# Kernel tuning notes

Hardware: AMD Instinct MI355X
Metric: run time of the kernel (lower is better)

Reference implementation:

```python
import jax, jax.numpy as jnp
import numpy as np


def setup_inputs() -> dict:
    key = jax.random.key(0)
    k1, k2, k3, k4 = jax.random.split(key, 4)
    B, T, C, H = 16, 2048, 384, 64
    x = jax.random.normal(k1, (B, T, C), dtype=jnp.float32)
    Wq = jax.random.normal(k2, (C, H), dtype=jnp.float32) * (1.0 / np.sqrt(C))
    Wk = jax.random.normal(k3, (C, H), dtype=jnp.float32) * (1.0 / np.sqrt(C))
    Wv = jax.random.normal(k4, (C, H), dtype=jnp.float32) * (1.0 / np.sqrt(C))
    return {"x": x, "Wq": Wq, "Wk": Wk, "Wv": Wv}


def reference(x, Wq, Wk, Wv):
    # x: [B, T, C]; Wq/Wk/Wv: [C, H]
    T = x.shape[1]
    H = Wk.shape[1]
    q = jnp.einsum('btc,ch->bth', x, Wq)
    k = jnp.einsum('btc,ch->bth', x, Wk)
    v = jnp.einsum('btc,ch->bth', x, Wv)
    scale = 1.0 / jnp.sqrt(jnp.asarray(H, dtype=x.dtype))
    wei = jnp.einsum('bth,bsh->bts', q, k) * scale  # [B, T, T]
    causal = jnp.tril(jnp.ones((T, T), dtype=bool))
    wei = jnp.where(causal, wei, -jnp.inf)
    attn = jax.nn.softmax(wei, axis=-1)
    # dropout p=0 -> identity
    out = jnp.einsum('bts,bsh->bth', attn, v)  # [B, T, H]
    return out
```

## Files before the change

kernel.cpp:

```cpp
#include <hip/hip_runtime.h>
#include <hip/hip_bf16.h>

#define B_ 16
#define T_ 2048
#define C_ 384
#define H_ 64

typedef __attribute__((ext_vector_type(8))) short short8;
typedef __attribute__((ext_vector_type(4))) short short4_t;
typedef __attribute__((ext_vector_type(4))) float floatx4;

static __device__ __forceinline__ short f2bf(float f) {
    unsigned u = __builtin_bit_cast(unsigned, f);
    u += 0x7FFF + ((u >> 16) & 1);
    return (short)(u >> 16);
}

__global__ void wt_kernel(const float* __restrict__ Wq, const float* __restrict__ Wk,
                          const float* __restrict__ Wv, short* __restrict__ wt2) {
    int idx = blockIdx.x * 256 + threadIdx.x;
    if (idx >= 12 * 12 * 512) return;
    int f = idx >> 9, within = idx & 511;
    int lane = within >> 3, jj = within & 7;
    int nt16 = f / 12, kc32 = f - nt16 * 12;
    int mat = nt16 >> 2, w = nt16 & 3;
    int quad = lane >> 4, l16 = lane & 15;
    int h = w * 16 + l16;
    int c = kc32 * 32 + quad * 8 + jj;
    const float* W = (mat == 0) ? Wq : ((mat == 1) ? Wk : Wv);
    wt2[idx] = f2bf(W[c * H_ + h]);
}

__global__ __launch_bounds__(256) void qkv_kernel(
        const float* __restrict__ x, const short* __restrict__ wt2,
        short* __restrict__ qo, short* __restrict__ ko, short* __restrict__ vto) {
    __shared__ short xs[32 * 392];

    int b = blockIdx.y, t0 = blockIdx.x * 32;
    int tid = threadIdx.x;

    const float* src = x + (size_t)(b * T_ + t0) * C_;
    for (int i = 0; i < 12; i++) {
        int chunk = i * 256 + tid;
        int row = chunk / 96, off = (chunk % 96) * 4;
        float4 f = *(const float4*)&src[row * 384 + off];
        short4_t s4;
        s4.x = f2bf(f.x); s4.y = f2bf(f.y); s4.z = f2bf(f.z); s4.w = f2bf(f.w);
        *(short4_t*)&xs[row * 392 + off] = s4;
    }
    __syncthreads();

    int w = tid >> 6, lane = tid & 63, quad = lane >> 4, l16 = lane & 15;

    floatx4 acc[2][3];
    for (int mt = 0; mt < 2; mt++)
        for (int j = 0; j < 3; j++) acc[mt][j] = (floatx4)0.0f;

    for (int kc = 0; kc < 384; kc += 32) {
        int kc32 = kc >> 5;
        short8 a0 = *(const short8*)&xs[l16 * 392 + kc + quad * 8];
        short8 a1 = *(const short8*)&xs[(16 + l16) * 392 + kc + quad * 8];
        for (int j = 0; j < 3; j++) {
            short8 bf = *(const short8*)&wt2[(((j * 4 + w) * 12) + kc32) * 512 + lane * 8];
            acc[0][j] = __builtin_amdgcn_mfma_f32_16x16x32_bf16(a0, bf, acc[0][j], 0, 0, 0);
            acc[1][j] = __builtin_amdgcn_mfma_f32_16x16x32_bf16(a1, bf, acc[1][j], 0, 0, 0);
        }
    }
    __syncthreads();

    {
        int h = w * 16 + l16;
        for (int j = 0; j < 3; j++)
            for (int mt = 0; mt < 2; mt++)
                for (int r = 0; r < 4; r++) {
                    int tl = mt * 16 + quad * 4 + r;
                    short bv = f2bf(acc[mt][j][r]);
                    if (j == 0)      xs[tl * 72 + h] = bv;
                    else if (j == 1) xs[2304 + tl * 72 + h] = bv;
                    else             xs[4608 + h * 40 + tl] = bv;
                }
    }
    __syncthreads();

    {
        int row = tid >> 3, off = (tid & 7) * 8;
        *(short8*)&qo[(size_t)(b * T_ + t0 + row) * H_ + off] = *(const short8*)&xs[row * 72 + off];
        *(short8*)&ko[(size_t)(b * T_ + t0 + row) * H_ + off] = *(const short8*)&xs[2304 + row * 72 + off];
    }
    {
        int h = tid >> 2, off = (tid & 3) * 8;
        *(short8*)&vto[(size_t)(b * H_ + h) * T_ + t0 + off] = *(const short8*)&xs[4608 + h * 40 + off];
    }
}

__global__ __launch_bounds__(256) void attn_seg_kernel(
        const short* __restrict__ q, const short* __restrict__ k,
        const short* __restrict__ vt, float* __restrict__ slots) {
    __shared__ short ks[64 * 72];
    __shared__ short vs[64 * 72];
    __shared__ short ps[128 * 72];

    int b = blockIdx.y, fid = blockIdx.x, nslot = gridDim.x;
    int tt = 0, cum = 0;
    while (cum + ((2 * tt + 5) >> 2) <= fid) { cum += (2 * tt + 5) >> 2; tt++; }
    int nk = 2 * tt + 2;
    int k0 = (fid - cum) * 4;
    int k1 = min(k0 + 4, nk);

    int tid = threadIdx.x, w = tid >> 6, lane = tid & 63, quad = lane >> 4, l16 = lane & 15;
    int trow0 = tt * 128 + w * 32;

    short8 aq[2][2];
    for (int mt = 0; mt < 2; mt++) {
        const short* qrow = q + (size_t)(b * T_ + trow0 + mt * 16 + l16) * H_;
        aq[mt][0] = *(const short8*)&qrow[quad * 8];
        aq[mt][1] = *(const short8*)&qrow[32 + quad * 8];
    }

    floatx4 o[2][4];
    float lp[2][4];
    for (int mt = 0; mt < 2; mt++)
        for (int i = 0; i < 4; i++) { o[mt][i] = (floatx4)0.0f; lp[mt][i] = 0.f; }

    const short* kb0 = k + (size_t)b * T_ * H_;
    const short* vtb = vt + (size_t)b * H_ * T_;
    short* psw = ps + w * 32 * 72;

    int srow = tid >> 3, soff = (tid & 7) * 8;
    const float C1 = 0.125f * 1.44269504f;
    const float C2 = 12.0f * 1.44269504f;

    for (int st = k0; st < k1; st++) {
        int s0 = st * 64;
        const short* kg = kb0 + (size_t)s0 * H_;
        const short* vg = vtb + s0;
        *(short8*)&ks[srow * 72 + soff]        = *(const short8*)&kg[srow * H_ + soff];
        *(short8*)&ks[(srow + 32) * 72 + soff] = *(const short8*)&kg[(srow + 32) * H_ + soff];
        *(short8*)&vs[srow * 72 + soff]        = *(const short8*)&vg[(size_t)srow * T_ + soff];
        *(short8*)&vs[(srow + 32) * 72 + soff] = *(const short8*)&vg[(size_t)(srow + 32) * T_ + soff];
        __syncthreads();

        floatx4 sacc[2][4];
        for (int mt = 0; mt < 2; mt++)
            for (int nt = 0; nt < 4; nt++) sacc[mt][nt] = (floatx4)0.0f;
        for (int nt = 0; nt < 4; nt++) {
            short8 bk0 = *(const short8*)&ks[(nt * 16 + l16) * 72 + quad * 8];
            short8 bk1 = *(const short8*)&ks[(nt * 16 + l16) * 72 + 32 + quad * 8];
            sacc[0][nt] = __builtin_amdgcn_mfma_f32_16x16x32_bf16(aq[0][0], bk0, sacc[0][nt], 0, 0, 0);
            sacc[0][nt] = __builtin_amdgcn_mfma_f32_16x16x32_bf16(aq[0][1], bk1, sacc[0][nt], 0, 0, 0);
            sacc[1][nt] = __builtin_amdgcn_mfma_f32_16x16x32_bf16(aq[1][0], bk0, sacc[1][nt], 0, 0, 0);
            sacc[1][nt] = __builtin_amdgcn_mfma_f32_16x16x32_bf16(aq[1][1], bk1, sacc[1][nt], 0, 0, 0);
        }

        bool diag = (st >= 2 * tt);
        for (int mt = 0; mt < 2; mt++)
            for (int nt = 0; nt < 4; nt++) {
                int s_idx = s0 + nt * 16 + l16;
                for (int r = 0; r < 4; r++) {
                    float p = exp2f(fmaf(sacc[mt][nt][r], C1, -C2));
                    if (diag && (s_idx > trow0 + mt * 16 + quad * 4 + r)) p = 0.0f;
                    lp[mt][r] += p;
                    psw[(mt * 16 + quad * 4 + r) * 72 + nt * 16 + l16] = f2bf(p);
                }
            }

        short8 ap[2][2];
        for (int mt = 0; mt < 2; mt++) {
            ap[mt][0] = *(const short8*)&psw[(mt * 16 + l16) * 72 + quad * 8];
            ap[mt][1] = *(const short8*)&psw[(mt * 16 + l16) * 72 + 32 + quad * 8];
        }
        for (int nh = 0; nh < 4; nh++) {
            short8 bv0 = *(const short8*)&vs[(nh * 16 + l16) * 72 + quad * 8];
            short8 bv1 = *(const short8*)&vs[(nh * 16 + l16) * 72 + 32 + quad * 8];
            o[0][nh] = __builtin_amdgcn_mfma_f32_16x16x32_bf16(ap[0][0], bv0, o[0][nh], 0, 0, 0);
            o[0][nh] = __builtin_amdgcn_mfma_f32_16x16x32_bf16(ap[0][1], bv1, o[0][nh], 0, 0, 0);
            o[1][nh] = __builtin_amdgcn_mfma_f32_16x16x32_bf16(ap[1][0], bv0, o[1][nh], 0, 0, 0);
            o[1][nh] = __builtin_amdgcn_mfma_f32_16x16x32_bf16(ap[1][1], bv1, o[1][nh], 0, 0, 0);
        }
        __syncthreads();
    }

    for (int d = 1; d < 16; d <<= 1)
        for (int mt = 0; mt < 2; mt++)
            for (int r = 0; r < 4; r++)
                lp[mt][r] += __shfl_xor(lp[mt][r], d, 16);

    float* slot = slots + ((size_t)b * nslot + fid) * 8320;
    for (int mt = 0; mt < 2; mt++)
        for (int nh = 0; nh < 4; nh++)
            for (int r = 0; r < 4; r++)
                slot[(w * 32 + mt * 16 + quad * 4 + r) * 64 + nh * 16 + l16] = o[mt][nh][r];
    if (l16 == 0)
        for (int mt = 0; mt < 2; mt++)
            for (int r = 0; r < 4; r++)
                slot[8192 + w * 32 + mt * 16 + quad * 4 + r] = lp[mt][r];
}

__global__ __launch_bounds__(256) void combine_kernel(
        const float* __restrict__ slots, int nslot, float* __restrict__ out) {
    int b = blockIdx.y, tt = blockIdx.x;
    int nseg = (2 * tt + 5) >> 2;
    int cum = 0;
    for (int i = 0; i < tt; i++) cum += (2 * i + 5) >> 2;
    const float* base = slots + ((size_t)b * nslot + cum) * 8320;

    int tid = threadIdx.x;
    int row = tid >> 1, c0 = (tid & 1) * 32;
    float4 acc[8] = {};
    float lsum = 0.f;
    for (int s = 0; s < nseg; s++) {
        const float* sp = base + (size_t)s * 8320;
        for (int i = 0; i < 8; i++) {
            float4 v = *(const float4*)&sp[row * 64 + c0 + i * 4];
            acc[i].x += v.x; acc[i].y += v.y; acc[i].z += v.z; acc[i].w += v.w;
        }
        lsum += sp[8192 + row];
    }
    float inv = 1.0f / lsum;
    float* op = out + (size_t)(b * T_ + tt * 128 + row) * H_ + c0;
    for (int i = 0; i < 8; i++) {
        float4 v;
        v.x = acc[i].x * inv; v.y = acc[i].y * inv;
        v.z = acc[i].z * inv; v.w = acc[i].w * inv;
        *(float4*)&op[i * 4] = v;
    }
}

template<bool DIAG>
static __device__ __forceinline__ void attn_step(
        int s0, int t0w, int quad, int l16,
        const short* __restrict__ kbase, const short* __restrict__ vtb,
        short8 aq0, short8 aq1, short* __restrict__ psw,
        floatx4 (&o)[4], float (&lpart)[4]) {
    floatx4 sacc[4];
    for (int nt = 0; nt < 4; nt++) sacc[nt] = (floatx4)0.0f;
    for (int nt = 0; nt < 4; nt++) {
        short8 bk0 = *(const short8*)&kbase[(nt * 16 + l16) * H_ + quad * 8];
        short8 bk1 = *(const short8*)&kbase[(nt * 16 + l16) * H_ + 32 + quad * 8];
        sacc[nt] = __builtin_amdgcn_mfma_f32_16x16x32_bf16(aq0, bk0, sacc[nt], 0, 0, 0);
        sacc[nt] = __builtin_amdgcn_mfma_f32_16x16x32_bf16(aq1, bk1, sacc[nt], 0, 0, 0);
    }
    const float C1 = 0.125f * 1.44269504f;
    const float C2 = 12.0f * 1.44269504f;
    for (int nt = 0; nt < 4; nt++) {
        int s_idx = s0 + nt * 16 + l16;
        for (int r = 0; r < 4; r++) {
            float p = exp2f(fmaf(sacc[nt][r], C1, -C2));
            if (DIAG && (s_idx > t0w + quad * 4 + r)) p = 0.0f;
            lpart[r] += p;
            psw[(quad * 4 + r) * 72 + nt * 16 + l16] = f2bf(p);
        }
    }
    short8 ap0 = *(const short8*)&psw[l16 * 72 + quad * 8];
    short8 ap1 = *(const short8*)&psw[l16 * 72 + 32 + quad * 8];
    for (int nh = 0; nh < 4; nh++) {
        short8 bv0 = *(const short8*)&vtb[(size_t)(nh * 16 + l16) * T_ + s0 + quad * 8];
        short8 bv1 = *(const short8*)&vtb[(size_t)(nh * 16 + l16) * T_ + s0 + 32 + quad * 8];
        o[nh] = __builtin_amdgcn_mfma_f32_16x16x32_bf16(ap0, bv0, o[nh], 0, 0, 0);
        o[nh] = __builtin_amdgcn_mfma_f32_16x16x32_bf16(ap1, bv1, o[nh], 0, 0, 0);
    }
}

__global__ __launch_bounds__(256) void attn_kernel(
        const short* __restrict__ q, const short* __restrict__ k,
        const short* __restrict__ vt, float* __restrict__ out) {
    __shared__ short ps[4 * 16 * 72];

    int b = blockIdx.y;
    int g = ((int)blockIdx.x + 4 * (b & 7)) & 31;
    int tt = (b < 8) ? g : 31 - g;
    int t0 = tt * 64;
    int tid = threadIdx.x, w = tid >> 6, lane = tid & 63, quad = lane >> 4, l16 = lane & 15;
    int t0w = t0 + w * 16;

    const short* qrow = q + (size_t)(b * T_ + t0w + l16) * H_;
    short8 aq0 = *(const short8*)&qrow[quad * 8];
    short8 aq1 = *(const short8*)&qrow[32 + quad * 8];

    floatx4 o[4];
    for (int nh = 0; nh < 4; nh++) o[nh] = (floatx4)0.0f;
    float lpart[4] = {0.f, 0.f, 0.f, 0.f};

    const short* kb0 = k + (size_t)b * T_ * H_;
    const short* vtb = vt + (size_t)b * H_ * T_;
    short* psw = ps + w * 16 * 72;

    for (int st = 0; st < tt; st++)
        attn_step<false>(st * 64, t0w, quad, l16, kb0 + (size_t)st * 64 * H_,
                         vtb, aq0, aq1, psw, o, lpart);
    attn_step<true>(tt * 64, t0w, quad, l16, kb0 + (size_t)tt * 64 * H_,
                    vtb, aq0, aq1, psw, o, lpart);

    for (int d = 1; d < 16; d <<= 1)
        for (int r = 0; r < 4; r++)
            lpart[r] += __shfl_xor(lpart[r], d, 16);

    for (int nh = 0; nh < 4; nh++)
        for (int r = 0; r < 4; r++) {
            int t = t0w + quad * 4 + r;
            out[(size_t)(b * T_ + t) * H_ + nh * 16 + l16] = o[nh][r] / lpart[r];
        }
}

extern "C" void kernel_launch(void* const* d_in, const int* in_sizes, int n_in,
                              void* d_out, int out_size, void* d_ws, size_t ws_size,
                              hipStream_t stream) {
    const float* x  = (const float*)d_in[0];
    const float* Wq = (const float*)d_in[1];
    const float* Wk = (const float*)d_in[2];
    const float* Wv = (const float*)d_in[3];

    char* ws = (char*)d_ws;
    short* qb  = (short*)(ws);
    short* kb  = (short*)(ws + (size_t)4 * 1024 * 1024);
    short* vtb = (short*)(ws + (size_t)8 * 1024 * 1024);
    short* wtb = (short*)(ws + (size_t)12 * 1024 * 1024);
    float* slots = (float*)(ws + (size_t)12 * 1024 * 1024 + 256 * 1024);
    size_t base_need = (size_t)12 * 1024 * 1024 + 256 * 1024;

    wt_kernel<<<dim3(288), dim3(256), 0, stream>>>(Wq, Wk, Wv, wtb);
    qkv_kernel<<<dim3(T_ / 32, B_), dim3(256), 0, stream>>>(x, wtb, qb, kb, vtb);

    float* out = (float*)d_out;
    const int NSLOT = 72;
    if (ws_size >= base_need + (size_t)B_ * NSLOT * 8320 * sizeof(float)) {
        attn_seg_kernel<<<dim3(NSLOT, B_), dim3(256), 0, stream>>>(qb, kb, vtb, slots);
        combine_kernel<<<dim3(T_ / 128, B_), dim3(256), 0, stream>>>(slots, NSLOT, out);
    } else {
        attn_kernel<<<dim3(T_ / 64, B_), dim3(256), 0, stream>>>(qb, kb, vtb, out);
    }
}
```

Measured before the change: 143.3 us.

## Double-buffer K/V tiles and store split-K partials as bf16

The segmented attention kernel now prefetches the next K/V tile into registers while computing the current one, then writes it into a second shared-memory buffer, removing one barrier per iteration. The per-warp P staging buffer is shrunk to 16 rows and reused per m-tile. Partial outputs in the slot buffer are stored as bf16 through shared memory with coalesced 16-byte stores instead of fp32, halving slot traffic for the combine kernel. This trades extra registers and some precision in the partial sums for less memory traffic and better load/compute overlap.

Measured after the change: 140.6 us. About the same (-1.9%).

```diff
diff --git a/kernel.cpp b/kernel.cpp
--- a/kernel.cpp
+++ b/kernel.cpp
@@ -14,6 +14,9 @@
     unsigned u = __builtin_bit_cast(unsigned, f);
     u += 0x7FFF + ((u >> 16) & 1);
     return (short)(u >> 16);
+}
+static __device__ __forceinline__ float bf2f(short s) {
+    return __builtin_bit_cast(float, ((unsigned)(unsigned short)s) << 16);
 }
 
 __global__ void wt_kernel(const float* __restrict__ Wq, const float* __restrict__ Wk,
@@ -93,12 +96,15 @@
     }
 }
 
+#define KVSZ (64 * 72)
+#define SLOT_BYTES (16384 + 512)
+
 __global__ __launch_bounds__(256) void attn_seg_kernel(
         const short* __restrict__ q, const short* __restrict__ k,
         const short* __restrict__ vt, float* __restrict__ slots) {
-    __shared__ short ks[64 * 72];
-    __shared__ short vs[64 * 72];
-    __shared__ short ps[128 * 72];
+    __shared__ short ks[2 * KVSZ];
+    __shared__ short vs[2 * KVSZ];
+    __shared__ short ps[4 * 16 * 72];
 
     int b = blockIdx.y, fid = blockIdx.x, nslot = gridDim.x;
     int tt = 0, cum = 0;
@@ -124,28 +130,48 @@
 
     const short* kb0 = k + (size_t)b * T_ * H_;
     const short* vtb = vt + (size_t)b * H_ * T_;
-    short* psw = ps + w * 32 * 72;
+    short* psw = ps + w * 16 * 72;
 
     int srow = tid >> 3, soff = (tid & 7) * 8;
     const float C1 = 0.125f * 1.44269504f;
     const float C2 = 12.0f * 1.44269504f;
 
+    {
+        const short* kg = kb0 + (size_t)k0 * 64 * H_;
+        const short* vg = vtb + k0 * 64;
+        short8 a = *(const short8*)&kg[srow * H_ + soff];
+        short8 c = *(const short8*)&kg[(srow + 32) * H_ + soff];
+        short8 d = *(const short8*)&vg[(size_t)srow * T_ + soff];
+        short8 e = *(const short8*)&vg[(size_t)(srow + 32) * T_ + soff];
+        *(short8*)&ks[srow * 72 + soff] = a;
+        *(short8*)&ks[(srow + 32) * 72 + soff] = c;
+        *(short8*)&vs[srow * 72 + soff] = d;
+        *(short8*)&vs[(srow + 32) * 72 + soff] = e;
+    }
+    __syncthreads();
+
+    int p = 0;
     for (int st = k0; st < k1; st++) {
+        bool more = (st + 1 < k1);
+        short8 pk0, pk1, pv0, pv1;
+        if (more) {
+            const short* kg = kb0 + (size_t)(st + 1) * 64 * H_;
+            const short* vg = vtb + (st + 1) * 64;
+            pk0 = *(const short8*)&kg[srow * H_ + soff];
+            pk1 = *(const short8*)&kg[(srow + 32) * H_ + soff];
+            pv0 = *(const short8*)&vg[(size_t)srow * T_ + soff];
+            pv1 = *(const short8*)&vg[(size_t)(srow + 32) * T_ + soff];
+        }
+        const short* ksp = ks + p * KVSZ;
+        const short* vsp = vs + p * KVSZ;
         int s0 = st * 64;
-        const short* kg = kb0 + (size_t)s0 * H_;
-        const short* vg = vtb + s0;
-        *(short8*)&ks[srow * 72 + soff]        = *(const short8*)&kg[srow * H_ + soff];
-        *(short8*)&ks[(srow + 32) * 72 + soff] = *(const short8*)&kg[(srow + 32) * H_ + soff];
-        *(short8*)&vs[srow * 72 + soff]        = *(const short8*)&vg[(size_t)srow * T_ + soff];
-        *(short8*)&vs[(srow + 32) * 72 + soff] = *(const short8*)&vg[(size_t)(srow + 32) * T_ + soff];
-        __syncthreads();
 
         floatx4 sacc[2][4];
         for (int mt = 0; mt < 2; mt++)
             for (int nt = 0; nt < 4; nt++) sacc[mt][nt] = (floatx4)0.0f;
         for (int nt = 0; nt < 4; nt++) {
-            short8 bk0 = *(const short8*)&ks[(nt * 16 + l16) * 72 + quad * 8];
-            short8 bk1 = *(const short8*)&ks[(nt * 16 + l16) * 72 + 32 + quad * 8];
+            short8 bk0 = *(const short8*)&ksp[(nt * 16 + l16) * 72 + quad * 8];
+            short8 bk1 = *(const short8*)&ksp[(nt * 16 + l16) * 72 + 32 + quad * 8];
             sacc[0][nt] = __builtin_amdgcn_mfma_f32_16x16x32_bf16(aq[0][0], bk0, sacc[0][nt], 0, 0, 0);
             sacc[0][nt] = __builtin_amdgcn_mfma_f32_16x16x32_bf16(aq[0][1], bk1, sacc[0][nt], 0, 0, 0);
             sacc[1][nt] = __builtin_amdgcn_mfma_f32_16x16x32_bf16(aq[1][0], bk0, sacc[1][nt], 0, 0, 0);
@@ -157,27 +183,41 @@
             for (int nt = 0; nt < 4; nt++) {
                 int s_idx = s0 + nt * 16 + l16;
                 for (int r = 0; r < 4; r++) {
-                    float p = exp2f(fmaf(sacc[mt][nt][r], C1, -C2));
-                    if (diag && (s_idx > trow0 + mt * 16 + quad * 4 + r)) p = 0.0f;
-                    lp[mt][r] += p;
-                    psw[(mt * 16 + quad * 4 + r) * 72 + nt * 16 + l16] = f2bf(p);
+                    float pv = exp2f(fmaf(sacc[mt][nt][r], C1, -C2));
+                    if (diag && (s_idx > trow0 + mt * 16 + quad * 4 + r)) pv = 0.0f;
+                    lp[mt][r] += pv;
+                    sacc[mt][nt][r] = pv;
                 }
             }
 
         short8 ap[2][2];
         for (int mt = 0; mt < 2; mt++) {
-            ap[mt][0] = *(const short8*)&psw[(mt * 16 + l16) * 72 + quad * 8];
-            ap[mt][1] = *(const short8*)&psw[(mt * 16 + l16) * 72 + 32 + quad * 8];
-        }
+            for (int nt = 0; nt < 4; nt++)
+                for (int r = 0; r < 4; r++)
+                    psw[(quad * 4 + r) * 72 + nt * 16 + l16] = f2bf(sacc[mt][nt][r]);
+            ap[mt][0] = *(const short8*)&psw[l16 * 72 + quad * 8];
+            ap[mt][1] = *(const short8*)&psw[l16 * 72 + 32 + quad * 8];
+        }
+
         for (int nh = 0; nh < 4; nh++) {
-            short8 bv0 = *(const short8*)&vs[(nh * 16 + l16) * 72 + quad * 8];
-            short8 bv1 = *(const short8*)&vs[(nh * 16 + l16) * 72 + 32 + quad * 8];
+            short8 bv0 = *(const short8*)&vsp[(nh * 16 + l16) * 72 + quad * 8];
+            short8 bv1 = *(const short8*)&vsp[(nh * 16 + l16) * 72 + 32 + quad * 8];
             o[0][nh] = __builtin_amdgcn_mfma_f32_16x16x32_bf16(ap[0][0], bv0, o[0][nh], 0, 0, 0);
             o[0][nh] = __builtin_amdgcn_mfma_f32_16x16x32_bf16(ap[0][1], bv1, o[0][nh], 0, 0, 0);
             o[1][nh] = __builtin_amdgcn_mfma_f32_16x16x32_bf16(ap[1][0], bv0, o[1][nh], 0, 0, 0);
             o[1][nh] = __builtin_amdgcn_mfma_f32_16x16x32_bf16(ap[1][1], bv1, o[1][nh], 0, 0, 0);
         }
-        __syncthreads();
+
+        if (more) {
+            short* kd = ks + (1 - p) * KVSZ;
+            short* vd = vs + (1 - p) * KVSZ;
+            *(short8*)&kd[srow * 72 + soff] = pk0;
+            *(short8*)&kd[(srow + 32) * 72 + soff] = pk1;
+            *(short8*)&vd[srow * 72 + soff] = pv0;
+            *(short8*)&vd[(srow + 32) * 72 + soff] = pv1;
+            __syncthreads();
+            p ^= 1;
+        }
     }
 
     for (int d = 1; d < 16; d <<= 1)
@@ -185,15 +225,25 @@
             for (int r = 0; r < 4; r++)
                 lp[mt][r] += __shfl_xor(lp[mt][r], d, 16);
 
-    float* slot = slots + ((size_t)b * nslot + fid) * 8320;
-    for (int mt = 0; mt < 2; mt++)
+    char* slotb = (char*)slots + ((size_t)b * nslot + fid) * SLOT_BYTES;
+    short* slotO = (short*)slotb;
+    float* slotL = (float*)(slotb + 16384);
+
+    for (int mt = 0; mt < 2; mt++) {
         for (int nh = 0; nh < 4; nh++)
             for (int r = 0; r < 4; r++)
-                slot[(w * 32 + mt * 16 + quad * 4 + r) * 64 + nh * 16 + l16] = o[mt][nh][r];
+                psw[(quad * 4 + r) * 72 + nh * 16 + l16] = f2bf(o[mt][nh][r]);
+        for (int it = 0; it < 2; it++) {
+            int u = it * 64 + lane;
+            int row = u >> 3, seg = u & 7;
+            *(short8*)&slotO[(w * 32 + mt * 16 + row) * 64 + seg * 8] =
+                *(const short8*)&psw[row * 72 + seg * 8];
+        }
+    }
     if (l16 == 0)
         for (int mt = 0; mt < 2; mt++)
             for (int r = 0; r < 4; r++)
-                slot[8192 + w * 32 + mt * 16 + quad * 4 + r] = lp[mt][r];
+                slotL[w * 32 + mt * 16 + quad * 4 + r] = lp[mt][r];
 }
 
 __global__ __launch_bounds__(256) void combine_kernel(
@@ -202,26 +252,28 @@
     int nseg = (2 * tt + 5) >> 2;
     int cum = 0;
     for (int i = 0; i < tt; i++) cum += (2 * i + 5) >> 2;
-    const float* base = slots + ((size_t)b * nslot + cum) * 8320;
+    const char* base = (const char*)slots + ((size_t)b * nslot + cum) * SLOT_BYTES;
 
     int tid = threadIdx.x;
-    int row = tid >> 1, c0 = (tid & 1) * 32;
-    float4 acc[8] = {};
+    int row = tid >> 1, half = tid & 1;
+    float acc[32];
+    for (int i = 0; i < 32; i++) acc[i] = 0.f;
     float lsum = 0.f;
     for (int s = 0; s < nseg; s++) {
-        const float* sp = base + (size_t)s * 8320;
-        for (int i = 0; i < 8; i++) {
-            float4 v = *(const float4*)&sp[row * 64 + c0 + i * 4];
-            acc[i].x += v.x; acc[i].y += v.y; acc[i].z += v.z; acc[i].w += v.w;
-        }
-        lsum += sp[8192 + row];
+        const short* O = (const short*)(base + (size_t)s * SLOT_BYTES);
+        const float* L = (const float*)(base + (size_t)s * SLOT_BYTES + 16384);
+        for (int i = 0; i < 4; i++) {
+            short8 v = *(const short8*)&O[row * 64 + half * 32 + i * 8];
+            for (int j = 0; j < 8; j++) acc[i * 8 + j] += bf2f(v[j]);
+        }
+        lsum += L[row];
     }
     float inv = 1.0f / lsum;
-    float* op = out + (size_t)(b * T_ + tt * 128 + row) * H_ + c0;
+    float* op = out + (size_t)(b * T_ + tt * 128 + row) * H_ + half * 32;
     for (int i = 0; i < 8; i++) {
         float4 v;
-        v.x = acc[i].x * inv; v.y = acc[i].y * inv;
-        v.z = acc[i].z * inv; v.w = acc[i].w * inv;
+        v.x = acc[i * 4 + 0] * inv; v.y = acc[i * 4 + 1] * inv;
+        v.z = acc[i * 4 + 2] * inv; v.w = acc[i * 4 + 3] * inv;
         *(float4*)&op[i * 4] = v;
     }
 }
@@ -323,7 +375,7 @@
 
     float* out = (float*)d_out;
     const int NSLOT = 72;
-    if (ws_size >= base_need + (size_t)B_ * NSLOT * 8320 * sizeof(float)) {
+    if (ws_size >= base_need + (size_t)B_ * NSLOT * (size_t)SLOT_BYTES) {
         attn_seg_kernel<<<dim3(NSLOT, B_), dim3(256), 0, stream>>>(qb, kb, vtb, slots);
         combine_kernel<<<dim3(T_ / 128, B_), dim3(256), 0, stream>>>(slots, NSLOT, out);
     } else {
```
